# Kernel tuning notes

Hardware: AMD Instinct MI355X
Metric: run time of the kernel (lower is better)

Reference implementation:

```python
import jax, jax.numpy as jnp
import numpy as np

B, N, E, H, ID = 32, 256, 512, 8, 8
D = E // H  # head dim = 64


def setup_inputs() -> dict:
    key = jax.random.key(0)
    ks = jax.random.split(key, 6)
    s = lambda k, shape, fan_in: jax.random.normal(k, shape, jnp.float32) * (fan_in ** -0.5)
    return {
        "x": jax.random.normal(ks[0], (B, N, E), jnp.float32),
        "U": jax.random.normal(ks[1], (B, N, N, ID), jnp.float32),
        "w_qkv": s(ks[2], (3 * E, E), E),   # nn.MultiheadAttention in_proj_weight
        "b_qkv": jnp.zeros((3 * E,), jnp.float32),
        "w_out": s(ks[3], (E, E), E),       # out_proj.weight
        "b_out": jnp.zeros((E,), jnp.float32),
        "w_u": s(ks[4], (H, ID), ID),       # u_proj.weight
        "b_u": jnp.zeros((H,), jnp.float32),
    }


def reference(x, U, w_qkv, b_qkv, w_out, b_out, w_u, b_u):
    # fused QKV projection (torch MHA uses a single in_proj)
    qkv = x @ w_qkv.T + b_qkv                      # [B,N,3E]
    q, k, v = jnp.split(qkv, 3, axis=-1)
    split_heads = lambda t: t.reshape(B, N, H, D).transpose(0, 2, 1, 3)  # [B,H,N,D]
    q, k, v = split_heads(q), split_heads(k), split_heads(v)
    # interaction tensor -> one additive bias per head: [B,N,N,H] -> [B,H,N,N]
    bias = (U @ w_u.T + b_u).transpose(0, 3, 1, 2)
    logits = jnp.einsum('bhnd,bhmd->bhnm', q, k) * (D ** -0.5) + bias  # [B,H,N,N]
    attn = jax.nn.softmax(logits, axis=-1)
    o = jnp.einsum('bhnm,bhmd->bhnd', attn, v)     # [B,H,N,D]
    o = o.transpose(0, 2, 1, 3).reshape(B, N, E)
    return o @ w_out.T + b_out
```

## Files before the change

kernel.cpp:

```cpp
#include <hip/hip_runtime.h>
#include <stdint.h>

#define Bn 32
#define Nn 256
#define En 512
#define Hn 8
#define Dn 64

typedef __attribute__((ext_vector_type(8))) short bf16x8;
typedef __attribute__((ext_vector_type(4))) short bf16x4;
typedef __attribute__((ext_vector_type(4))) float f32x4;

__device__ __forceinline__ unsigned short f2bf(float f){
  union{float f; uint32_t i;} v; v.f = f;
  uint32_t i = v.i;
  return (unsigned short)((i + 0x7fffu + ((i>>16)&1u)) >> 16);
}

__global__ __launch_bounds__(256) void convert_x(
    const float* __restrict__ x, unsigned short* __restrict__ xb){
  size_t i = ((size_t)blockIdx.x * 256 + threadIdx.x) * 8;
  float4 a = *(const float4*)(x + i);
  float4 b = *(const float4*)(x + i + 4);
  bf16x8 p;
  p[0]=(short)f2bf(a.x); p[1]=(short)f2bf(a.y); p[2]=(short)f2bf(a.z); p[3]=(short)f2bf(a.w);
  p[4]=(short)f2bf(b.x); p[5]=(short)f2bf(b.y); p[6]=(short)f2bf(b.z); p[7]=(short)f2bf(b.w);
  *(bf16x8*)(xb + i) = p;
}

__global__ __launch_bounds__(256) void qkv_gemm(
    const unsigned short* __restrict__ xb, const float* __restrict__ wq,
    const float* __restrict__ bq,
    unsigned short* __restrict__ q_ws, unsigned short* __restrict__ k_ws,
    unsigned short* __restrict__ v_ws){
  __shared__ unsigned short s_a[128][40];
  __shared__ unsigned short s_b[128][40];
  const int tid = threadIdx.x;
  const int bx = blockIdx.x;
  const int by = blockIdx.y;
  const int row0 = by * 128, n0 = bx * 128;
  const int lane = tid & 63, wv = tid >> 6;
  const int wr = wv >> 1, wc = wv & 1;
  const int lm = lane & 15, quad = lane >> 4;
  const int sr = tid >> 3, sc4 = (tid & 7) * 4;
  f32x4 acc[4][4] = {};
  for (int kc = 0; kc < 16; ++kc) {
    const int k0 = kc * 32;
    __syncthreads();
    #pragma unroll
    for (int i = 0; i < 2; ++i) {
      int g = tid * 2 + i;
      int r = g >> 2, c8 = (g & 3) * 8;
      *(bf16x8*)&s_a[r][c8] = *(const bf16x8*)(xb + (size_t)(row0 + r)*512 + k0 + c8);
    }
    #pragma unroll
    for (int i = 0; i < 4; ++i) {
      int r = sr + i * 32;
      float4 vb = *(const float4*)(wq + (size_t)(n0 + r) * 512 + k0 + sc4);
      bf16x4 pb;
      pb[0]=(short)f2bf(vb.x); pb[1]=(short)f2bf(vb.y); pb[2]=(short)f2bf(vb.z); pb[3]=(short)f2bf(vb.w);
      *(bf16x4*)&s_b[r][sc4] = pb;
    }
    __syncthreads();
    bf16x8 af[4], bfr[4];
    #pragma unroll
    for (int mt = 0; mt < 4; ++mt) af[mt]  = *(const bf16x8*)&s_a[wr*64 + mt*16 + lm][quad*8];
    #pragma unroll
    for (int nt = 0; nt < 4; ++nt) bfr[nt] = *(const bf16x8*)&s_b[wc*64 + nt*16 + lm][quad*8];
    #pragma unroll
    for (int mt = 0; mt < 4; ++mt)
      #pragma unroll
      for (int nt = 0; nt < 4; ++nt)
        acc[mt][nt] = __builtin_amdgcn_mfma_f32_16x16x32_bf16(af[mt], bfr[nt], acc[mt][nt], 0, 0, 0);
  }
  #pragma unroll
  for (int nt = 0; nt < 4; ++nt) {
    int c = n0 + wc*64 + nt*16 + lm;
    float bias = bq[c];
    int sec = c >> 9, ch = c & 511, h = ch >> 6, d = ch & 63;
    #pragma unroll
    for (int mt = 0; mt < 4; ++mt) {
      #pragma unroll
      for (int r = 0; r < 4; ++r) {
        int grow = row0 + wr*64 + mt*16 + quad*4 + r;
        int b = grow >> 8, n = grow & 255;
        float val = acc[mt][nt][r] + bias;
        if (sec == 0)      q_ws[(((size_t)b*Hn + h)*Nn + n)*Dn + d] = f2bf(val * 0.125f);
        else if (sec == 1) k_ws[(((size_t)b*Hn + h)*Nn + n)*Dn + d] = f2bf(val);
        else               v_ws[(((size_t)b*Hn + h)*Dn + d)*Nn + n] = f2bf(val);
      }
    }
  }
}

__global__ __launch_bounds__(256) void attn_kernel(
    const float* __restrict__ U, const float* __restrict__ w_u, const float* __restrict__ b_u,
    const unsigned short* __restrict__ q_ws, const unsigned short* __restrict__ k_ws,
    const unsigned short* __restrict__ v_ws, unsigned short* __restrict__ o_ws){
  __shared__ unsigned short s_p[4][2][16][40];
  __shared__ float s_wu[64];
  __shared__ float s_bu[8];
  const int tid = threadIdx.x;
  const int wv = tid >> 6, lane = tid & 63;
  const int lm = lane & 15, quad = lane >> 4;
  const int blk = blockIdx.x;
  const int b = blk >> 4, qt0 = (blk & 15) * 16;
  if (tid < 64) s_wu[tid] = w_u[tid];
  if (tid < 8)  s_bu[tid] = b_u[tid];
  __syncthreads();
  const int h0 = wv * 2, h1 = h0 + 1;
  const size_t hb0 = (size_t)b * Hn + h0, hb1 = hb0 + 1;
  float wu0[8], wu1[8];
  #pragma unroll
  for (int i = 0; i < 8; ++i) { wu0[i] = s_wu[h0*8 + i]; wu1[i] = s_wu[h1*8 + i]; }
  const float bu0 = s_bu[h0], bu1 = s_bu[h1];
  const unsigned short* q0p = q_ws + (hb0*Nn + qt0 + lm)*Dn;
  const unsigned short* q1p = q_ws + (hb1*Nn + qt0 + lm)*Dn;
  const bf16x8 qa0 = *(const bf16x8*)(q0p + quad*8);
  const bf16x8 qa1 = *(const bf16x8*)(q0p + 32 + quad*8);
  const bf16x8 qb0 = *(const bf16x8*)(q1p + quad*8);
  const bf16x8 qb1 = *(const bf16x8*)(q1p + 32 + quad*8);
  f32x4 oa[4] = {}, ob[4] = {};
  float m0[4], m1[4], l0[4], l1[4];
  #pragma unroll
  for (int r = 0; r < 4; ++r) { m0[r] = m1[r] = -3.0e38f; l0[r] = l1[r] = 0.f; }
  const float* Ub = U + ((size_t)(b*Nn + qt0)) * Nn * 8;
  #pragma unroll 1
  for (int ck = 0; ck < 8; ++ck) {
    f32x4 la0, la1, lb0, lb1;
    #pragma unroll
    for (int t = 0; t < 2; ++t) {
      const int key0 = ck*32 + t*16;
      f32x4 c0, c1;
      #pragma unroll
      for (int r = 0; r < 4; ++r) {
        const float4* up = (const float4*)(Ub + ((size_t)(quad*4+r)*Nn + key0 + lm)*8);
        float4 ua = up[0], uc = up[1];
        c0[r] = bu0 + ua.x*wu0[0] + ua.y*wu0[1] + ua.z*wu0[2] + ua.w*wu0[3]
                    + uc.x*wu0[4] + uc.y*wu0[5] + uc.z*wu0[6] + uc.w*wu0[7];
        c1[r] = bu1 + ua.x*wu1[0] + ua.y*wu1[1] + ua.z*wu1[2] + ua.w*wu1[3]
                    + uc.x*wu1[4] + uc.y*wu1[5] + uc.z*wu1[6] + uc.w*wu1[7];
      }
      const unsigned short* k0p = k_ws + (hb0*Nn + key0 + lm)*Dn;
      const unsigned short* k1p = k_ws + (hb1*Nn + key0 + lm)*Dn;
      bf16x8 kf;
      kf = *(const bf16x8*)(k0p + quad*8);
      c0 = __builtin_amdgcn_mfma_f32_16x16x32_bf16(qa0, kf, c0, 0, 0, 0);
      kf = *(const bf16x8*)(k0p + 32 + quad*8);
      c0 = __builtin_amdgcn_mfma_f32_16x16x32_bf16(qa1, kf, c0, 0, 0, 0);
      kf = *(const bf16x8*)(k1p + quad*8);
      c1 = __builtin_amdgcn_mfma_f32_16x16x32_bf16(qb0, kf, c1, 0, 0, 0);
      kf = *(const bf16x8*)(k1p + 32 + quad*8);
      c1 = __builtin_amdgcn_mfma_f32_16x16x32_bf16(qb1, kf, c1, 0, 0, 0);
      if (t == 0) { la0 = c0; lb0 = c1; } else { la1 = c0; lb1 = c1; }
    }
    #pragma unroll
    for (int r = 0; r < 4; ++r) {
      {
        float tm = fmaxf(la0[r], la1[r]);
        #pragma unroll
        for (int msk = 1; msk < 16; msk <<= 1) tm = fmaxf(tm, __shfl_xor(tm, msk));
        float mn = fmaxf(m0[r], tm);
        float al = __expf(m0[r] - mn);
        m0[r] = mn;
        float e0 = __expf(la0[r] - mn), e1 = __expf(la1[r] - mn);
        la0[r] = e0; la1[r] = e1;
        float s = e0 + e1;
        #pragma unroll
        for (int msk = 1; msk < 16; msk <<= 1) s += __shfl_xor(s, msk);
        l0[r] = l0[r] * al + s;
        #pragma unroll
        for (int nt = 0; nt < 4; ++nt) oa[nt][r] *= al;
      }
      {
        float tm = fmaxf(lb0[r], lb1[r]);
        #pragma unroll
        for (int msk = 1; msk < 16; msk <<= 1) tm = fmaxf(tm, __shfl_xor(tm, msk));
        float mn = fmaxf(m1[r], tm);
        float al = __expf(m1[r] - mn);
        m1[r] = mn;
        float e0 = __expf(lb0[r] - mn), e1 = __expf(lb1[r] - mn);
        lb0[r] = e0; lb1[r] = e1;
        float s = e0 + e1;
        #pragma unroll
        for (int msk = 1; msk < 16; msk <<= 1) s += __shfl_xor(s, msk);
        l1[r] = l1[r] * al + s;
        #pragma unroll
        for (int nt = 0; nt < 4; ++nt) ob[nt][r] *= al;
      }
    }
    #pragma unroll
    for (int r = 0; r < 4; ++r) {
      s_p[wv][0][quad*4+r][lm]      = f2bf(la0[r]);
      s_p[wv][0][quad*4+r][16 + lm] = f2bf(la1[r]);
      s_p[wv][1][quad*4+r][lm]      = f2bf(lb0[r]);
      s_p[wv][1][quad*4+r][16 + lm] = f2bf(lb1[r]);
    }
    const bf16x8 ap0 = *(const bf16x8*)&s_p[wv][0][lm][quad*8];
    const bf16x8 ap1 = *(const bf16x8*)&s_p[wv][1][lm][quad*8];
    #pragma unroll
    for (int nt = 0; nt < 4; ++nt) {
      bf16x8 bv = *(const bf16x8*)(v_ws + (hb0*Dn + nt*16 + lm)*Nn + ck*32 + quad*8);
      oa[nt] = __builtin_amdgcn_mfma_f32_16x16x32_bf16(ap0, bv, oa[nt], 0, 0, 0);
      bv = *(const bf16x8*)(v_ws + (hb1*Dn + nt*16 + lm)*Nn + ck*32 + quad*8);
      ob[nt] = __builtin_amdgcn_mfma_f32_16x16x32_bf16(ap1, bv, ob[nt], 0, 0, 0);
    }
  }
  #pragma unroll
  for (int r = 0; r < 4; ++r) {
    const float i0 = 1.0f / l0[r], i1 = 1.0f / l1[r];
    const int n = qt0 + quad*4 + r;
    #pragma unroll
    for (int nt = 0; nt < 4; ++nt) {
      o_ws[((size_t)(b*Nn + n))*En + h0*64 + nt*16 + lm] = f2bf(oa[nt][r] * i0);
      o_ws[((size_t)(b*Nn + n))*En + h1*64 + nt*16 + lm] = f2bf(ob[nt][r] * i1);
    }
  }
}

__global__ __launch_bounds__(256) void oproj_gemm(
    const unsigned short* __restrict__ o_ws, const float* __restrict__ wo,
    const float* __restrict__ bo, float* __restrict__ out){
  __shared__ unsigned short s_a[128][40];
  __shared__ unsigned short s_b[128][40];
  const int tid = threadIdx.x;
  const int bx = blockIdx.x;
  const int by = blockIdx.y;
  const int row0 = by * 128, n0 = bx * 128;
  const int lane = tid & 63, wv = tid >> 6;
  const int wr = wv >> 1, wc = wv & 1;
  const int lm = lane & 15, quad = lane >> 4;
  const int sr = tid >> 3, sc4 = (tid & 7) * 4;
  f32x4 acc[4][4] = {};
  for (int kc = 0; kc < 16; ++kc) {
    const int k0 = kc * 32;
    __syncthreads();
    #pragma unroll
    for (int i = 0; i < 2; ++i) {
      int g = tid * 2 + i;
      int r = g >> 2, c8 = (g & 3) * 8;
      *(bf16x8*)&s_a[r][c8] = *(const bf16x8*)(o_ws + (size_t)(row0 + r)*512 + k0 + c8);
    }
    #pragma unroll
    for (int i = 0; i < 4; ++i) {
      int r = sr + i * 32;
      float4 vb = *(const float4*)(wo + (size_t)(n0 + r) * 512 + k0 + sc4);
      bf16x4 pb;
      pb[0]=(short)f2bf(vb.x); pb[1]=(short)f2bf(vb.y); pb[2]=(short)f2bf(vb.z); pb[3]=(short)f2bf(vb.w);
      *(bf16x4*)&s_b[r][sc4] = pb;
    }
    __syncthreads();
    bf16x8 af[4], bfr[4];
    #pragma unroll
    for (int mt = 0; mt < 4; ++mt) af[mt]  = *(const bf16x8*)&s_a[wr*64 + mt*16 + lm][quad*8];
    #pragma unroll
    for (int nt = 0; nt < 4; ++nt) bfr[nt] = *(const bf16x8*)&s_b[wc*64 + nt*16 + lm][quad*8];
    #pragma unroll
    for (int mt = 0; mt < 4; ++mt)
      #pragma unroll
      for (int nt = 0; nt < 4; ++nt)
        acc[mt][nt] = __builtin_amdgcn_mfma_f32_16x16x32_bf16(af[mt], bfr[nt], acc[mt][nt], 0, 0, 0);
  }
  #pragma unroll
  for (int nt = 0; nt < 4; ++nt) {
    int c = n0 + wc*64 + nt*16 + lm;
    float bias = bo[c];
    #pragma unroll
    for (int mt = 0; mt < 4; ++mt)
      #pragma unroll
      for (int r = 0; r < 4; ++r) {
        int grow = row0 + wr*64 + mt*16 + quad*4 + r;
        out[(size_t)grow*512 + c] = acc[mt][nt][r] + bias;
      }
  }
}

extern "C" void kernel_launch(void* const* d_in, const int* in_sizes, int n_in,
                              void* d_out, int out_size, void* d_ws, size_t ws_size,
                              hipStream_t stream) {
  const float* x     = (const float*)d_in[0];
  const float* U     = (const float*)d_in[1];
  const float* w_qkv = (const float*)d_in[2];
  const float* b_qkv = (const float*)d_in[3];
  const float* w_out = (const float*)d_in[4];
  const float* b_out = (const float*)d_in[5];
  const float* w_u   = (const float*)d_in[6];
  const float* b_u   = (const float*)d_in[7];
  float* out = (float*)d_out;

  const size_t per = (size_t)Bn * Hn * Nn * Dn;
  unsigned short* q_ws = (unsigned short*)d_ws;
  unsigned short* k_ws = q_ws + per;
  unsigned short* v_ws = k_ws + per;
  unsigned short* o_ws = v_ws + per;

  convert_x <<<dim3(2048),  dim3(256), 0, stream>>>(x, o_ws);
  qkv_gemm  <<<dim3(12, 64), dim3(256), 0, stream>>>(o_ws, w_qkv, b_qkv, q_ws, k_ws, v_ws);
  attn_kernel<<<dim3(Bn * 16), dim3(256), 0, stream>>>(U, w_u, b_u, q_ws, k_ws, v_ws, o_ws);
  oproj_gemm<<<dim3(4, 64), dim3(256), 0, stream>>>(o_ws, w_out, b_out, out);
}
```

Measured before the change: 220.9 us.

## Precompute fp16 interaction bias in prep kernel and use lean attention kernel

Merges the x-to-bf16 conversion with a new pass that projects U into a per-head fp16 bias tensor, written in the MFMA accumulator tile order. A new attention kernel loads that bias straight into the QK accumulator, handles one head per wave with an online softmax over 32-key chunks, and uses a grid ordering that groups blocks by batch and head pair. The aim is to take the U projection out of the attention inner loop and shrink its per-block work. The cost is an extra 32 MB of workspace traffic, fp16 precision on the bias, and a fallback to the old path when the workspace is too small.

```diff
diff --git a/kernel.cpp b/kernel.cpp
--- a/kernel.cpp
+++ b/kernel.cpp
@@ -10,6 +10,7 @@
 typedef __attribute__((ext_vector_type(8))) short bf16x8;
 typedef __attribute__((ext_vector_type(4))) short bf16x4;
 typedef __attribute__((ext_vector_type(4))) float f32x4;
+typedef __attribute__((ext_vector_type(4))) _Float16 h4f;
 
 __device__ __forceinline__ unsigned short f2bf(float f){
   union{float f; uint32_t i;} v; v.f = f;
@@ -26,6 +27,60 @@
   p[0]=(short)f2bf(a.x); p[1]=(short)f2bf(a.y); p[2]=(short)f2bf(a.z); p[3]=(short)f2bf(a.w);
   p[4]=(short)f2bf(b.x); p[5]=(short)f2bf(b.y); p[6]=(short)f2bf(b.z); p[7]=(short)f2bf(b.w);
   *(bf16x8*)(xb + i) = p;
+}
+
+__global__ __launch_bounds__(256) void prep_kernel(
+    const float* __restrict__ x, unsigned short* __restrict__ xb,
+    const float* __restrict__ U, const float* __restrict__ w_u,
+    const float* __restrict__ b_u, unsigned short* __restrict__ bias16){
+  __shared__ float s_wu[64];
+  __shared__ float s_bu[8];
+  const int bx = blockIdx.x;
+  const int tid = threadIdx.x;
+  if (bx < 2048) {
+    size_t i = ((size_t)bx * 256 + tid) * 8;
+    float4 a = *(const float4*)(x + i);
+    float4 b = *(const float4*)(x + i + 4);
+    bf16x8 p;
+    p[0]=(short)f2bf(a.x); p[1]=(short)f2bf(a.y); p[2]=(short)f2bf(a.z); p[3]=(short)f2bf(a.w);
+    p[4]=(short)f2bf(b.x); p[5]=(short)f2bf(b.y); p[6]=(short)f2bf(b.z); p[7]=(short)f2bf(b.w);
+    *(bf16x8*)(xb + i) = p;
+    return;
+  }
+  if (tid < 64) s_wu[tid] = w_u[tid];
+  if (tid < 8)  s_bu[tid] = b_u[tid];
+  __syncthreads();
+  const int t  = (bx - 2048) * 256 + tid;
+  const int m_ = t & 255;
+  const int n4 = (t >> 8) & 63;
+  const int bb = t >> 14;
+  const float* up = U + ((size_t)(bb*Nn + n4*4)*Nn + m_) * 8;
+  float u[4][8];
+  #pragma unroll
+  for (int r = 0; r < 4; ++r) {
+    float4 a = *(const float4*)(up + (size_t)r * (Nn*8));
+    float4 c = *(const float4*)(up + (size_t)r * (Nn*8) + 4);
+    u[r][0]=a.x; u[r][1]=a.y; u[r][2]=a.z; u[r][3]=a.w;
+    u[r][4]=c.x; u[r][5]=c.y; u[r][6]=c.z; u[r][7]=c.w;
+  }
+  const int    lane_in = ((n4 & 3) * 16 + (m_ & 15)) * 4;
+  const size_t tbase   = ((size_t)(n4 >> 2) * 16 + (m_ >> 4)) * 256;
+  #pragma unroll
+  for (int h = 0; h < 8; ++h) {
+    const float bu = s_bu[h];
+    float acc[4];
+    #pragma unroll
+    for (int r = 0; r < 4; ++r) {
+      float a = bu;
+      #pragma unroll
+      for (int id = 0; id < 8; ++id) a += u[r][id] * s_wu[h*8 + id];
+      acc[r] = a;
+    }
+    h4f hv;
+    hv[0]=(_Float16)acc[0]; hv[1]=(_Float16)acc[1];
+    hv[2]=(_Float16)acc[2]; hv[3]=(_Float16)acc[3];
+    *(h4f*)(bias16 + (size_t)(bb*Hn + h) * 65536 + tbase + lane_in) = hv;
+  }
 }
 
 __global__ __launch_bounds__(256) void qkv_gemm(
@@ -90,6 +145,83 @@
         else               v_ws[(((size_t)b*Hn + h)*Dn + d)*Nn + n] = f2bf(val);
       }
     }
+  }
+}
+
+__global__ __launch_bounds__(256) void attn_fast(
+    const unsigned short* __restrict__ bias16,
+    const unsigned short* __restrict__ q_ws, const unsigned short* __restrict__ k_ws,
+    const unsigned short* __restrict__ v_ws, unsigned short* __restrict__ o_ws){
+  __shared__ unsigned short s_p[4][16][40];
+  const int tid = threadIdx.x;
+  const int wv = tid >> 6, lane = tid & 63;
+  const int lm = lane & 15, quad = lane >> 4;
+  const int bx = blockIdx.x;
+  const int g  = (bx & 7) * 8 + ((bx >> 3) >> 4);
+  const int qt = (bx >> 3) & 15;
+  const int b = g >> 1, hp = g & 1;
+  const int h = hp * 4 + wv;
+  const size_t hb = (size_t)b * Hn + h;
+  const int qt0 = qt * 16;
+  const unsigned short* qp = q_ws + (hb*Nn + qt0 + lm) * Dn;
+  const bf16x8 qa0 = *(const bf16x8*)(qp + quad*8);
+  const bf16x8 qa1 = *(const bf16x8*)(qp + 32 + quad*8);
+  const unsigned short* bt = bias16 + (hb*16 + qt) * 16 * 256 + (size_t)lane*4;
+  f32x4 oa[4] = {};
+  float m0[4], l0[4];
+  #pragma unroll
+  for (int r = 0; r < 4; ++r) { m0[r] = -3.0e38f; l0[r] = 0.f; }
+  #pragma unroll 1
+  for (int ck = 0; ck < 8; ++ck) {
+    f32x4 la0, la1;
+    #pragma unroll
+    for (int t = 0; t < 2; ++t) {
+      const int key0 = ck*32 + t*16;
+      const h4f hv = *(const h4f*)(bt + (ck*2 + t) * 256);
+      f32x4 c0;
+      #pragma unroll
+      for (int r = 0; r < 4; ++r) c0[r] = (float)hv[r];
+      const unsigned short* kp = k_ws + (hb*Nn + key0 + lm) * Dn;
+      c0 = __builtin_amdgcn_mfma_f32_16x16x32_bf16(qa0, *(const bf16x8*)(kp + quad*8),      c0, 0, 0, 0);
+      c0 = __builtin_amdgcn_mfma_f32_16x16x32_bf16(qa1, *(const bf16x8*)(kp + 32 + quad*8), c0, 0, 0, 0);
+      if (t == 0) la0 = c0; else la1 = c0;
+    }
+    #pragma unroll
+    for (int r = 0; r < 4; ++r) {
+      float tm = fmaxf(la0[r], la1[r]);
+      #pragma unroll
+      for (int msk = 1; msk < 16; msk <<= 1) tm = fmaxf(tm, __shfl_xor(tm, msk));
+      float mn = fmaxf(m0[r], tm);
+      float al = __expf(m0[r] - mn);
+      m0[r] = mn;
+      float e0 = __expf(la0[r] - mn), e1 = __expf(la1[r] - mn);
+      la0[r] = e0; la1[r] = e1;
+      float s = e0 + e1;
+      #pragma unroll
+      for (int msk = 1; msk < 16; msk <<= 1) s += __shfl_xor(s, msk);
+      l0[r] = l0[r] * al + s;
+      #pragma unroll
+      for (int nt = 0; nt < 4; ++nt) oa[nt][r] *= al;
+    }
+    #pragma unroll
+    for (int r = 0; r < 4; ++r) {
+      s_p[wv][quad*4+r][lm]      = f2bf(la0[r]);
+      s_p[wv][quad*4+r][16 + lm] = f2bf(la1[r]);
+    }
+    const bf16x8 ap = *(const bf16x8*)&s_p[wv][lm][quad*8];
+    #pragma unroll
+    for (int nt = 0; nt < 4; ++nt) {
+      const bf16x8 bv = *(const bf16x8*)(v_ws + (hb*Dn + nt*16 + lm)*Nn + ck*32 + quad*8);
+      oa[nt] = __builtin_amdgcn_mfma_f32_16x16x32_bf16(ap, bv, oa[nt], 0, 0, 0);
+    }
+  }
+  #pragma unroll
+  for (int r = 0; r < 4; ++r) {
+    const float inv = 1.0f / l0[r];
+    const int n = qt0 + quad*4 + r;
+    #pragma unroll
+    for (int nt = 0; nt < 4; ++nt)
+      o_ws[((size_t)(b*Nn + n))*En + h*64 + nt*16 + lm] = f2bf(oa[nt][r] * inv);
   }
 }
 
@@ -293,9 +425,19 @@
   unsigned short* k_ws = q_ws + per;
   unsigned short* v_ws = k_ws + per;
   unsigned short* o_ws = v_ws + per;
-
-  convert_x <<<dim3(2048),  dim3(256), 0, stream>>>(x, o_ws);
-  qkv_gemm  <<<dim3(12, 64), dim3(256), 0, stream>>>(o_ws, w_qkv, b_qkv, q_ws, k_ws, v_ws);
-  attn_kernel<<<dim3(Bn * 16), dim3(256), 0, stream>>>(U, w_u, b_u, q_ws, k_ws, v_ws, o_ws);
-  oproj_gemm<<<dim3(4, 64), dim3(256), 0, stream>>>(o_ws, w_out, b_out, out);
-}
+  unsigned short* bias16 = o_ws + per;
+
+  const size_t need = per * 2 * 4 + (size_t)Bn * Hn * Nn * Nn * 2;
+
+  if (ws_size >= need) {
+    prep_kernel<<<dim3(4096),  dim3(256), 0, stream>>>(x, o_ws, U, w_u, b_u, bias16);
+    qkv_gemm  <<<dim3(12, 64), dim3(256), 0, stream>>>(o_ws, w_qkv, b_qkv, q_ws, k_ws, v_ws);
+    attn_fast <<<dim3(1024),   dim3(256), 0, stream>>>(bias16, q_ws, k_ws, v_ws, o_ws);
+    oproj_gemm<<<dim3(4, 64),  dim3(256), 0, stream>>>(o_ws, w_out, b_out, out);
+  } else {
+    convert_x <<<dim3(2048),  dim3(256), 0, stream>>>(x, o_ws);
+    qkv_gemm  <<<dim3(12, 64), dim3(256), 0, stream>>>(o_ws, w_qkv, b_qkv, q_ws, k_ws, v_ws);
+    attn_kernel<<<dim3(Bn * 16), dim3(256), 0, stream>>>(U, w_u, b_u, q_ws, k_ws, v_ws, o_ws);
+    oproj_gemm<<<dim3(4, 64), dim3(256), 0, stream>>>(o_ws, w_out, b_out, out);
+  }
+}
```

New measurement: 219.8 us. No clear change (-0.5%).
